# Kernel tuning notes

Hardware: AMD Instinct MI355X
Metric: run time of the kernel (lower is better)

Reference implementation:

```python
import jax, jax.numpy as jnp
import numpy as np

B, S, D, H = 2, 2048, 1024, 16
HD = D // H


def _linear_params(key, scale):
    kw, kb = jax.random.split(key)
    W = jax.random.normal(kw, (D, D), dtype=jnp.float32) * scale
    b = jax.random.normal(kb, (D,), dtype=jnp.float32) * scale
    return W, b


def setup_inputs() -> dict:
    key = jax.random.key(0)
    keys = jax.random.split(key, 10)
    scale = 1.0 / np.sqrt(D)
    vis = jax.random.normal(keys[0], (B, S, D), dtype=jnp.float32)
    inf = jax.random.normal(keys[1], (B, S, D), dtype=jnp.float32)
    names = ["q_vis", "k_vis", "v_vis", "q_inf", "k_inf", "v_inf", "o_vis", "o_inf"]
    out = {"vis": vis, "inf": inf}
    for n, k in zip(names, keys[2:]):
        W, b = _linear_params(k, scale)
        out["W_" + n] = W
        out["b_" + n] = b
    return out


def _heads(x):
    # [B,S,D] -> [B,H,S,HD]
    return x.reshape(B, S, H, HD).transpose(0, 2, 1, 3)


def _merge(x):
    # [B,H,S,HD] -> [B,S,D]
    return x.transpose(0, 2, 1, 3).reshape(B, S, D)


def reference(vis, inf, W_q_vis, b_q_vis, W_k_vis, b_k_vis, W_v_vis, b_v_vis,
              W_q_inf, b_q_inf, W_k_inf, b_k_inf, W_v_inf, b_v_inf,
              W_o_vis, b_o_vis, W_o_inf, b_o_inf):
    Qv = _heads(vis @ W_q_vis + b_q_vis)
    Kv = _heads(vis @ W_k_vis + b_k_vis)
    Vv = _heads(vis @ W_v_vis + b_v_vis)
    Qi = _heads(inf @ W_q_inf + b_q_inf)
    Ki = _heads(inf @ W_k_inf + b_k_inf)
    Vi = _heads(inf @ W_v_inf + b_v_inf)
    scale = 1.0 / jnp.sqrt(jnp.float32(HD))
    # vis queries attend over inf keys/values
    scores_vi = jnp.einsum("bhqd,bhkd->bhqk", Qv, Ki) * scale
    attn_inf = jax.nn.softmax(scores_vi, axis=-1)
    out_inf = jnp.einsum("bhqk,bhkd->bhqd", attn_inf, Vi)
    # inf queries attend over vis keys/values
    scores_iv = jnp.einsum("bhqd,bhkd->bhqk", Qi, Kv) * scale
    attn_vis = jax.nn.softmax(scores_iv, axis=-1)
    out_vis = jnp.einsum("bhqk,bhkd->bhqd", attn_vis, Vv)
    out_vis = _merge(out_vis) @ W_o_vis + b_o_vis
    out_inf = _merge(out_inf) @ W_o_inf + b_o_inf
    return (out_vis, out_inf)
```

## Files before the change

kernel.cpp:

```cpp
#include <hip/hip_runtime.h>
#include <hip/hip_bf16.h>

#define DEV __device__ __forceinline__

typedef __attribute__((ext_vector_type(4))) float f32x4;
typedef __attribute__((ext_vector_type(16))) float f32x16;
typedef __attribute__((ext_vector_type(8))) __bf16 bf16x8;
typedef __attribute__((ext_vector_type(8))) unsigned short ushort8;
typedef __attribute__((ext_vector_type(4))) unsigned int uint32x4;

static constexpr int BATCH = 2, SEQ = 2048, DM = 1024, NH = 16, HDIM = 64;
static constexpr size_t XSZ = (size_t)BATCH * SEQ * DM;

DEV unsigned short f2bf(float f) {
  union { float f; unsigned int u; } v; v.f = f;
  unsigned int r = (v.u + 0x7fffu + ((v.u >> 16) & 1u)) >> 16;
  return (unsigned short)r;
}

DEV bf16x8 ld8(const unsigned short* p) {
  return __builtin_bit_cast(bf16x8, *(const ushort8*)p);
}

DEV f32x4 mfma16(bf16x8 a, bf16x8 b, f32x4 c) {
  return __builtin_amdgcn_mfma_f32_16x16x32_bf16(a, b, c, 0, 0, 0);
}
DEV f32x16 mfma32(bf16x8 a, bf16x8 b, f32x16 c) {
  return __builtin_amdgcn_mfma_f32_32x32x16_bf16(a, b, c, 0, 0, 0);
}

DEV unsigned cvtpk(float lo, float hi) {
  unsigned r;
  asm("v_cvt_pk_bf16_f32 %0, %1, %2" : "=v"(r) : "v"(lo), "v"(hi));
  return r;
}
DEV void plswap(unsigned& a, unsigned& b) {
  asm("v_permlane32_swap_b32 %0, %1" : "+v"(a), "+v"(b));
}

DEV void gll16(const unsigned short* g, unsigned short* l) {
  __builtin_amdgcn_global_load_lds(
      (__attribute__((address_space(1))) void*)(unsigned short*)g,
      (__attribute__((address_space(3))) void*)l, 16, 0, 0);
}

__global__ __launch_bounds__(256)
void k_convert_x(const float* __restrict__ vis, const float* __restrict__ inff,
                 unsigned short* __restrict__ out) {
  const float* src = blockIdx.z ? inff : vis;
  unsigned short* dst = out + (size_t)blockIdx.z * XSZ;
  const size_t i = ((size_t)blockIdx.x * 256 + threadIdx.x) * 8;
  const float4 a = *(const float4*)(src + i);
  const float4 b = *(const float4*)(src + i + 4);
  ushort8 v;
  v[0] = f2bf(a.x); v[1] = f2bf(a.y); v[2] = f2bf(a.z); v[3] = f2bf(a.w);
  v[4] = f2bf(b.x); v[5] = f2bf(b.y); v[6] = f2bf(b.z); v[7] = f2bf(b.w);
  *(ushort8*)(dst + i) = v;
}

struct WPtrs { const float* w[8]; };

__global__ __launch_bounds__(256)
void k_convert_w(WPtrs p, unsigned short* __restrict__ wt) {
  const float* W = p.w[blockIdx.z];
  unsigned short* Wt = wt + (size_t)blockIdx.z * (1024 * 1024);
  const int k0 = blockIdx.y * 64, n0 = blockIdx.x * 64;
  __shared__ unsigned short t[64][68];
  const int tx = threadIdx.x & 15, ty = threadIdx.x >> 4;
#pragma unroll
  for (int i = 0; i < 4; ++i) {
    const int kr = ty * 4 + i;
    const float4 v = *(const float4*)(W + (size_t)(k0 + kr) * 1024 + n0 + tx * 4);
    t[kr][tx * 4 + 0] = f2bf(v.x); t[kr][tx * 4 + 1] = f2bf(v.y);
    t[kr][tx * 4 + 2] = f2bf(v.z); t[kr][tx * 4 + 3] = f2bf(v.w);
  }
  __syncthreads();
#pragma unroll
  for (int i = 0; i < 4; ++i) {
    const int nr = ty * 4 + i;
    ushort4 o;
    o.x = t[tx * 4 + 0][nr]; o.y = t[tx * 4 + 1][nr];
    o.z = t[tx * 4 + 2][nr]; o.w = t[tx * 4 + 3][nr];
    *(ushort4*)(Wt + (size_t)(n0 + nr) * 1024 + k0 + tx * 4) = o;
  }
}

struct GemmJob { const unsigned short* A; const unsigned short* W;
                 const float* bias; void* out; float scale; int mode; };
struct GemmJobs { GemmJob j[6]; };

__global__ __launch_bounds__(256)
void k_gemm(GemmJobs jobs) {
  const GemmJob jb = jobs.j[blockIdx.z];
  const int lane = threadIdx.x & 63, w = threadIdx.x >> 6;
  const int wr = w >> 1, wc = w & 1;
  const int r = lane & 15, g = lane >> 4;

  const int nid = blockIdx.x + (blockIdx.y << 3);
  const int bxs = nid >> 5;
  const int bys = ((nid & 7) << 2) + ((nid >> 3) & 3);
  const int bm = bys * 128, bn = bxs * 128;

  __shared__ __align__(16) unsigned short As[128 * 64];
  __shared__ __align__(16) unsigned short Bs[128 * 64];

  const int srow = lane >> 3;
  const int schunk = (lane & 7) ^ srow;
  const unsigned short* Ag = jb.A + (size_t)(bm + w * 32 + srow) * DM + schunk * 8;
  const unsigned short* Bg = jb.W + (size_t)(bn + w * 32 + srow) * DM + schunk * 8;

  f32x4 acc[4][4] = {};

  for (int kt = 0; kt < DM; kt += 64) {
#pragma unroll
    for (int j = 0; j < 4; ++j) {
      gll16(Ag + kt + j * 8 * DM, As + (w * 4 + j) * 512);
      gll16(Bg + kt + j * 8 * DM, Bs + (w * 4 + j) * 512);
    }
    __syncthreads();
#pragma unroll
    for (int kk = 0; kk < 2; ++kk) {
      bf16x8 a[4], b[4];
#pragma unroll
      for (int m = 0; m < 4; ++m) {
        const int row = wr * 64 + m * 16 + r;
        const int pos = (kk * 4 + g) ^ (row & 7);
        a[m] = ld8(As + row * 64 + pos * 8);
      }
#pragma unroll
      for (int n = 0; n < 4; ++n) {
        const int row = wc * 64 + n * 16 + r;
        const int pos = (kk * 4 + g) ^ (row & 7);
        b[n] = ld8(Bs + row * 64 + pos * 8);
      }
#pragma unroll
      for (int m = 0; m < 4; ++m)
#pragma unroll
        for (int n = 0; n < 4; ++n)
          acc[m][n] = mfma16(a[m], b[n], acc[m][n]);
    }
    __syncthreads();
  }

  if (jb.mode == 0) {
    unsigned short* O = (unsigned short*)jb.out;
#pragma unroll
    for (int n = 0; n < 4; ++n) {
      const int nc = bn + wc * 64 + n * 16 + r;
      const float bv = jb.bias[nc];
      const int h = nc >> 6, hd = nc & 63;
#pragma unroll
      for (int m = 0; m < 4; ++m)
#pragma unroll
        for (int i = 0; i < 4; ++i) {
          const int mr = bm + wr * 64 + m * 16 + g * 4 + i;
          const int bb = mr >> 11, s = mr & 2047;
          O[((size_t)(bb * NH + h) * SEQ + s) * HDIM + hd] =
              f2bf((acc[m][n][i] + bv) * jb.scale);
        }
    }
  } else if (jb.mode == 2) {
    unsigned short* O = (unsigned short*)jb.out;
#pragma unroll
    for (int n = 0; n < 4; ++n) {
      const int nc = bn + wc * 64 + n * 16 + r;
      const float bv = jb.bias[nc];
      const int h = nc >> 6, hd = nc & 63;
#pragma unroll
      for (int m = 0; m < 4; ++m) {
        const int mr = bm + wr * 64 + m * 16 + g * 4;
        const int bb = mr >> 11, s = mr & 2047;
        ushort4 pv;
        pv.x = f2bf(acc[m][n][0] + bv);
        pv.y = f2bf(acc[m][n][1] + bv);
        pv.z = f2bf(acc[m][n][2] + bv);
        pv.w = f2bf(acc[m][n][3] + bv);
        *(ushort4*)(O + ((size_t)(bb * NH + h) * HDIM + hd) * SEQ + s) = pv;
      }
    }
  } else {
    float* O = (float*)jb.out;
#pragma unroll
    for (int n = 0; n < 4; ++n) {
      const int nc = bn + wc * 64 + n * 16 + r;
      const float bv = jb.bias[nc];
#pragma unroll
      for (int m = 0; m < 4; ++m)
#pragma unroll
        for (int i = 0; i < 4; ++i) {
          const int mr = bm + wr * 64 + m * 16 + g * 4 + i;
          O[(size_t)mr * DM + nc] = acc[m][n][i] + bv;
        }
    }
  }
}

struct AttnJob { const unsigned short* Q; const unsigned short* K;
                 const unsigned short* Vt; unsigned short* O; };
struct AttnJobs { AttnJob j[2]; };

__global__ __launch_bounds__(512, 4)
void k_attn(AttnJobs jobs) {
  const AttnJob jb = jobs.j[blockIdx.z];
  const int nid = blockIdx.x + (blockIdx.y << 3);
  const int qt = nid >> 5;
  const int bh = ((nid & 7) << 2) + ((nid >> 3) & 3);
  const int lane = threadIdx.x & 63, w = threadIdx.x >> 6;
  const int q5 = lane & 31, hi = lane >> 5;
  const int qrow = qt * 256 + w * 32 + q5;

  const unsigned short* Qp = jb.Q + (size_t)bh * SEQ * HDIM;
  const unsigned short* Kp = jb.K + (size_t)bh * SEQ * HDIM;
  const unsigned short* Vp = jb.Vt + (size_t)bh * HDIM * SEQ;

  __shared__ __align__(16) unsigned short Ks[3][64 * 64];
  __shared__ __align__(16) unsigned short Vs[3][64 * 64];

  bf16x8 qf[4];
#pragma unroll
  for (int c = 0; c < 4; ++c)
    qf[c] = ld8(Qp + (size_t)qrow * HDIM + c * 16 + hi * 8);

  const int srow = w * 8 + (lane >> 3);
  const int schunk = (lane & 7) ^ (srow & 7);
  const unsigned short* Kg = Kp + (size_t)srow * HDIM + schunk * 8;
  const unsigned short* Vg = Vp + (size_t)srow * SEQ + schunk * 8;

  auto stage = [&](int buf, int kv0) {
    gll16(Kg + (size_t)kv0 * HDIM, Ks[buf] + w * 512);
    gll16(Vg + kv0,                Vs[buf] + w * 512);
  };

  f32x16 o0 = {}, o1 = {};
  float mrow = -1e30f, lrow = 0.f;
  const int swz = q5 & 7;
  constexpr int NT = SEQ / 64;

  stage(0, 0);
  stage(1, 64);
  asm volatile("s_waitcnt vmcnt(2)" ::: "memory");
  __builtin_amdgcn_s_barrier();
  __builtin_amdgcn_sched_barrier(0);

  int cur = 0, sb = 2;
  for (int t = 0; t < NT; ++t) {
    if (t + 2 < NT) stage(sb, (t + 2) * 64);

    f32x16 s0 = {}, s1 = {};
    __builtin_amdgcn_s_setprio(1);
#pragma unroll
    for (int c = 0; c < 4; ++c) {
      const int sl = ((2 * c + hi) ^ swz) * 8;
      s0 = mfma32(ld8(Ks[cur] + q5 * 64 + sl), qf[c], s0);
      s1 = mfma32(ld8(Ks[cur] + (32 + q5) * 64 + sl), qf[c], s1);
    }
    __builtin_amdgcn_s_setprio(0);

    float tm[8];
#pragma unroll
    for (int r = 0; r < 8; ++r)
      tm[r] = fmaxf(fmaxf(s0[r], s0[r + 8]), fmaxf(s1[r], s1[r + 8]));
    float mx = fmaxf(fmaxf(fmaxf(tm[0], tm[1]), tm[2]),
                     fmaxf(fmaxf(tm[3], tm[4]), fmaxf(fmaxf(tm[5], tm[6]), tm[7])));
    mx = fmaxf(mx, __shfl_xor(mx, 32, 64));

    if (!__all(mx <= mrow + 11.5416f)) {
      const float mn = fmaxf(mx, mrow);
      const float al = __builtin_amdgcn_exp2f(mrow - mn);
      mrow = mn;
      lrow *= al;
#pragma unroll
      for (int r = 0; r < 16; ++r) { o0[r] *= al; o1[r] *= al; }
    }

    float ps0 = 0.f, ps1 = 0.f;
#pragma unroll
    for (int r = 0; r < 16; ++r) {
      s0[r] = __builtin_amdgcn_exp2f(s0[r] - mrow); ps0 += s0[r];
      s1[r] = __builtin_amdgcn_exp2f(s1[r] - mrow); ps1 += s1[r];
    }
    lrow += ps0 + ps1;

    unsigned pk0[8], pk1[8];
#pragma unroll
    for (int ww = 0; ww < 8; ++ww) {
      pk0[ww] = cvtpk(s0[2 * ww], s0[2 * ww + 1]);
      pk1[ww] = cvtpk(s1[2 * ww], s1[2 * ww + 1]);
    }

    __builtin_amdgcn_s_setprio(1);
#pragma unroll
    for (int c = 0; c < 4; ++c) {
      const int wb = 4 * (c & 1);
      unsigned a0 = (c < 2) ? pk0[wb + 0] : pk1[wb + 0];
      unsigned a1 = (c < 2) ? pk0[wb + 1] : pk1[wb + 1];
      unsigned b0 = (c < 2) ? pk0[wb + 2] : pk1[wb + 2];
      unsigned b1 = (c < 2) ? pk0[wb + 3] : pk1[wb + 3];
      plswap(a0, b0);
      plswap(a1, b1);
      uint32x4 fw = {a0, a1, b0, b1};
      const bf16x8 pf = __builtin_bit_cast(bf16x8, fw);
      const int sl = ((2 * c + hi) ^ swz) * 8;
      o0 = mfma32(ld8(Vs[cur] + q5 * 64 + sl), pf, o0);
      o1 = mfma32(ld8(Vs[cur] + (32 + q5) * 64 + sl), pf, o1);
    }
    __builtin_amdgcn_s_setprio(0);

    if (t + 1 < NT) {
      if (t + 2 < NT) {
        asm volatile("s_waitcnt vmcnt(2)" ::: "memory");
      } else {
        asm volatile("s_waitcnt vmcnt(0)" ::: "memory");
      }
      __builtin_amdgcn_s_barrier();
      __builtin_amdgcn_sched_barrier(0);
    }
    sb = cur;
    cur = (cur == 2) ? 0 : cur + 1;
  }

  const float ltot = lrow + __shfl_xor(lrow, 32, 64);
  const float inv = 1.f / ltot;
  const int bb = bh >> 4, h = bh & 15;
  unsigned short* Ob = jb.O + ((size_t)bb * SEQ + qrow) * DM + h * HDIM;

  auto storeO = [&](const f32x16 oo, int dbase) {
#pragma unroll
    for (int g4 = 0; g4 < 4; ++g4) {
      ushort4 pv;
      pv.x = f2bf(oo[4 * g4 + 0] * inv);
      pv.y = f2bf(oo[4 * g4 + 1] * inv);
      pv.z = f2bf(oo[4 * g4 + 2] * inv);
      pv.w = f2bf(oo[4 * g4 + 3] * inv);
      *(ushort4*)(Ob + dbase + 8 * g4 + 4 * hi) = pv;
    }
  };
  storeO(o0, 0);
  storeO(o1, 32);
}

extern "C" void kernel_launch(void* const* d_in, const int* in_sizes, int n_in,
                              void* d_out, int out_size, void* d_ws, size_t ws_size,
                              hipStream_t stream) {
  const float* vis = (const float*)d_in[0];
  const float* inff = (const float*)d_in[1];

  unsigned short* xbf  = (unsigned short*)d_ws;
  unsigned short* wt   = xbf + 2 * XSZ;
  unsigned short* Qv   = wt + (size_t)8 * 1024 * 1024;
  unsigned short* Kv   = Qv + XSZ;
  unsigned short* Vv   = Kv + XSZ;
  unsigned short* Qi   = Vv + XSZ;
  unsigned short* Ki   = Qi + XSZ;
  unsigned short* Vi   = Ki + XSZ;
  unsigned short* Vvt  = Vi + XSZ;
  unsigned short* Vit  = Vvt + XSZ;
  unsigned short* atA  = Vit + XSZ;
  unsigned short* atB  = atA + XSZ;

  k_convert_x<<<dim3(2048, 1, 2), 256, 0, stream>>>(vis, inff, xbf);

  WPtrs wp;
  wp.w[0] = (const float*)d_in[2];  wp.w[1] = (const float*)d_in[4];
  wp.w[2] = (const float*)d_in[6];  wp.w[3] = (const float*)d_in[8];
  wp.w[4] = (const float*)d_in[10]; wp.w[5] = (const float*)d_in[12];
  wp.w[6] = (const float*)d_in[14]; wp.w[7] = (const float*)d_in[16];
  k_convert_w<<<dim3(16, 16, 8), 256, 0, stream>>>(wp, wt);

  const size_t WSZ = (size_t)1024 * 1024;
  const float qsc = 0.18033688011f;
  GemmJobs pj;
  pj.j[0] = { xbf,       wt + 0 * WSZ, (const float*)d_in[3],  (void*)Qv,  qsc, 0 };
  pj.j[1] = { xbf,       wt + 1 * WSZ, (const float*)d_in[5],  (void*)Kv,  1.f, 0 };
  pj.j[2] = { xbf,       wt + 2 * WSZ, (const float*)d_in[7],  (void*)Vvt, 1.f, 2 };
  pj.j[3] = { xbf + XSZ, wt + 3 * WSZ, (const float*)d_in[9],  (void*)Qi,  qsc, 0 };
  pj.j[4] = { xbf + XSZ, wt + 4 * WSZ, (const float*)d_in[11], (void*)Ki,  1.f, 0 };
  pj.j[5] = { xbf + XSZ, wt + 5 * WSZ, (const float*)d_in[13], (void*)Vit, 1.f, 2 };
  k_gemm<<<dim3(8, 32, 6), 256, 0, stream>>>(pj);

  AttnJobs aj;
  aj.j[0] = { Qv, Ki, Vit, atA };
  aj.j[1] = { Qi, Kv, Vvt, atB };
  k_attn<<<dim3(8, 32, 2), 512, 0, stream>>>(aj);

  GemmJobs oj;
  oj.j[0] = { atB, wt + 6 * WSZ, (const float*)d_in[15], d_out, 1.f, 1 };
  oj.j[1] = { atA, wt + 7 * WSZ, (const float*)d_in[17], (void*)((float*)d_out + XSZ), 1.f, 1 };
  for (int z = 2; z < 6; ++z) oj.j[z] = oj.j[0];
  k_gemm<<<dim3(8, 32, 2), 256, 0, stream>>>(oj);
}
```

Before: 303.8 us.

## Replace GEMM with 256x256-tile double-buffered pipelined kernel and grid swizzle

The 128x128 single-buffered GEMM (256 threads) is replaced by a 256x256-tile kernel with 512 threads and two LDS buffers for each operand half. The next K-tile's loads are staged during compute, and each 64-wide K step is split into four phases separated by barriers and raised MFMA priority. A new block-index swizzle spreads jobs across the grid. This aims for more data reuse and overlap of global loads with MFMA, but the grid shrinks to 384 blocks for the projections and 128 for the output GEMM, which may underfill the CUs, and the register pressure from the accumulators rises.

```diff
diff --git a/kernel.cpp b/kernel.cpp
--- a/kernel.cpp
+++ b/kernel.cpp
@@ -89,57 +89,98 @@
                  const float* bias; void* out; float scale; int mode; };
 struct GemmJobs { GemmJob j[6]; };
 
-__global__ __launch_bounds__(256)
-void k_gemm(GemmJobs jobs) {
-  const GemmJob jb = jobs.j[blockIdx.z];
+__global__ __launch_bounds__(512, 2)
+void k_gemm256(GemmJobs jobs) {
   const int lane = threadIdx.x & 63, w = threadIdx.x >> 6;
-  const int wr = w >> 1, wc = w & 1;
+  const int wr = w >> 2, wc = w & 3;
   const int r = lane & 15, g = lane >> 4;
 
-  const int nid = blockIdx.x + (blockIdx.y << 3);
-  const int bxs = nid >> 5;
-  const int bys = ((nid & 7) << 2) + ((nid >> 3) & 3);
-  const int bm = bys * 128, bn = bxs * 128;
-
-  __shared__ __align__(16) unsigned short As[128 * 64];
-  __shared__ __align__(16) unsigned short Bs[128 * 64];
-
-  const int srow = lane >> 3;
-  const int schunk = (lane & 7) ^ srow;
-  const unsigned short* Ag = jb.A + (size_t)(bm + w * 32 + srow) * DM + schunk * 8;
-  const unsigned short* Bg = jb.W + (size_t)(bn + w * 32 + srow) * DM + schunk * 8;
-
-  f32x4 acc[4][4] = {};
-
-  for (int kt = 0; kt < DM; kt += 64) {
-#pragma unroll
-    for (int j = 0; j < 4; ++j) {
-      gll16(Ag + kt + j * 8 * DM, As + (w * 4 + j) * 512);
-      gll16(Bg + kt + j * 8 * DM, Bs + (w * 4 + j) * 512);
-    }
-    __syncthreads();
-#pragma unroll
-    for (int kk = 0; kk < 2; ++kk) {
-      bf16x8 a[4], b[4];
-#pragma unroll
-      for (int m = 0; m < 4; ++m) {
-        const int row = wr * 64 + m * 16 + r;
-        const int pos = (kk * 4 + g) ^ (row & 7);
-        a[m] = ld8(As + row * 64 + pos * 8);
-      }
-#pragma unroll
-      for (int n = 0; n < 4; ++n) {
-        const int row = wc * 64 + n * 16 + r;
-        const int pos = (kk * 4 + g) ^ (row & 7);
-        b[n] = ld8(Bs + row * 64 + pos * 8);
-      }
-#pragma unroll
-      for (int m = 0; m < 4; ++m)
-#pragma unroll
-        for (int n = 0; n < 4; ++n)
-          acc[m][n] = mfma16(a[m], b[n], acc[m][n]);
-    }
-    __syncthreads();
+  const int lin = blockIdx.x + (blockIdx.y << 2) + ((blockIdx.z * 16) << 2);
+  const int q = gridDim.z << 3;
+  const int swz = (lin & 7) * q + (lin >> 3);
+  const int bxs = swz & 3, bys = (swz >> 2) & 15, bzs = swz >> 6;
+  const GemmJob jb = jobs.j[bzs];
+  const int bm = bys * 256, bn = bxs * 256;
+
+  __shared__ __align__(16) unsigned short L[2][2][2][8192];
+
+  const int uu = ((lane & 7) ^ (lane >> 3)) * 8;
+  const int rb = w * 8 + (lane >> 3);
+
+  auto stage = [&](int d_, int ab, int h, int tt) {
+#pragma unroll
+    for (int j = 0; j < 2; ++j) {
+      const int R = h * 128 + j * 64 + rb;
+      const unsigned short* src = (ab ? jb.W : jb.A)
+          + (size_t)((ab ? bn : bm) + R) * DM + tt * 64 + uu;
+      gll16(src, &L[d_][ab][h][(j * 8 + w) * 512]);
+    }
+  };
+
+  f32x4 acc[8][4] = {};
+  constexpr int NKT = DM / 64;
+
+  stage(0, 0, 0, 0); stage(0, 0, 1, 0); stage(0, 1, 0, 0); stage(0, 1, 1, 0);
+  stage(1, 1, 0, 1); stage(1, 1, 1, 1);
+  asm volatile("s_waitcnt vmcnt(4)" ::: "memory");
+  __builtin_amdgcn_s_barrier();
+  __builtin_amdgcn_sched_barrier(0);
+
+  const int px0 = (g ^ (r & 7)) * 8, px1 = ((4 + g) ^ (r & 7)) * 8;
+
+  for (int t = 0; t < NKT; ++t) {
+    const int d = t & 1;
+    const unsigned short* Ab = &L[d][0][wr][0];
+    const unsigned short* Bb = &L[d][1][wc >> 1][0];
+    bf16x8 bfr[4][2];
+
+#pragma unroll
+    for (int p = 0; p < 4; ++p) {
+      if (p == 0) {
+#pragma unroll
+        for (int n = 0; n < 4; ++n) {
+          const int rowl = (wc & 1) * 64 + n * 16 + r;
+          bfr[n][0] = ld8(Bb + rowl * 64 + px0);
+          bfr[n][1] = ld8(Bb + rowl * 64 + px1);
+        }
+      }
+      bf16x8 af[2][2];
+#pragma unroll
+      for (int m2 = 0; m2 < 2; ++m2) {
+        const int rowl = (2 * p + m2) * 16 + r;
+        af[m2][0] = ld8(Ab + rowl * 64 + px0);
+        af[m2][1] = ld8(Ab + rowl * 64 + px1);
+      }
+      if (p == 0 && t + 1 < NKT) stage(d ^ 1, 0, 0, t + 1);
+      if (p == 1 && t + 1 < NKT) stage(d ^ 1, 0, 1, t + 1);
+      if (p == 2 && t + 2 < NKT) stage(d, 1, 0, t + 2);
+      if (p == 3 && t + 2 < NKT) stage(d, 1, 1, t + 2);
+
+      __builtin_amdgcn_s_barrier();
+      asm volatile("s_waitcnt lgkmcnt(0)" ::: "memory");
+      __builtin_amdgcn_sched_barrier(0);
+
+      __builtin_amdgcn_s_setprio(1);
+#pragma unroll
+      for (int m2 = 0; m2 < 2; ++m2) {
+        const int mm = 2 * p + m2;
+#pragma unroll
+        for (int n = 0; n < 4; ++n) {
+          acc[mm][n] = mfma16(af[m2][0], bfr[n][0], acc[mm][n]);
+          acc[mm][n] = mfma16(af[m2][1], bfr[n][1], acc[mm][n]);
+        }
+      }
+      __builtin_amdgcn_s_setprio(0);
+
+      if (p < 3) {
+        __builtin_amdgcn_s_barrier();
+      } else if (t + 1 < NKT) {
+        if (t + 2 < NKT) asm volatile("s_waitcnt vmcnt(4)" ::: "memory");
+        else             asm volatile("s_waitcnt vmcnt(0)" ::: "memory");
+        __builtin_amdgcn_s_barrier();
+        __builtin_amdgcn_sched_barrier(0);
+      }
+    }
   }
 
   if (jb.mode == 0) {
@@ -150,10 +191,10 @@
       const float bv = jb.bias[nc];
       const int h = nc >> 6, hd = nc & 63;
 #pragma unroll
-      for (int m = 0; m < 4; ++m)
+      for (int m = 0; m < 8; ++m)
 #pragma unroll
         for (int i = 0; i < 4; ++i) {
-          const int mr = bm + wr * 64 + m * 16 + g * 4 + i;
+          const int mr = bm + wr * 128 + m * 16 + g * 4 + i;
           const int bb = mr >> 11, s = mr & 2047;
           O[((size_t)(bb * NH + h) * SEQ + s) * HDIM + hd] =
               f2bf((acc[m][n][i] + bv) * jb.scale);
@@ -167,8 +208,8 @@
       const float bv = jb.bias[nc];
       const int h = nc >> 6, hd = nc & 63;
 #pragma unroll
-      for (int m = 0; m < 4; ++m) {
-        const int mr = bm + wr * 64 + m * 16 + g * 4;
+      for (int m = 0; m < 8; ++m) {
+        const int mr = bm + wr * 128 + m * 16 + g * 4;
         const int bb = mr >> 11, s = mr & 2047;
         ushort4 pv;
         pv.x = f2bf(acc[m][n][0] + bv);
@@ -185,10 +226,10 @@
       const int nc = bn + wc * 64 + n * 16 + r;
       const float bv = jb.bias[nc];
 #pragma unroll
-      for (int m = 0; m < 4; ++m)
+      for (int m = 0; m < 8; ++m)
 #pragma unroll
         for (int i = 0; i < 4; ++i) {
-          const int mr = bm + wr * 64 + m * 16 + g * 4 + i;
+          const int mr = bm + wr * 128 + m * 16 + g * 4 + i;
           O[(size_t)mr * DM + nc] = acc[m][n][i] + bv;
         }
     }
@@ -233,7 +274,7 @@
 
   f32x16 o0 = {}, o1 = {};
   float mrow = -1e30f, lrow = 0.f;
-  const int swz = q5 & 7;
+  const int swzl = q5 & 7;
   constexpr int NT = SEQ / 64;
 
   stage(0, 0);
@@ -250,7 +291,7 @@
     __builtin_amdgcn_s_setprio(1);
 #pragma unroll
     for (int c = 0; c < 4; ++c) {
-      const int sl = ((2 * c + hi) ^ swz) * 8;
+      const int sl = ((2 * c + hi) ^ swzl) * 8;
       s0 = mfma32(ld8(Ks[cur] + q5 * 64 + sl), qf[c], s0);
       s1 = mfma32(ld8(Ks[cur] + (32 + q5) * 64 + sl), qf[c], s1);
     }
@@ -258,8 +299,8 @@
 
     float tm[8];
 #pragma unroll
-    for (int r = 0; r < 8; ++r)
-      tm[r] = fmaxf(fmaxf(s0[r], s0[r + 8]), fmaxf(s1[r], s1[r + 8]));
+    for (int rr = 0; rr < 8; ++rr)
+      tm[rr] = fmaxf(fmaxf(s0[rr], s0[rr + 8]), fmaxf(s1[rr], s1[rr + 8]));
     float mx = fmaxf(fmaxf(fmaxf(tm[0], tm[1]), tm[2]),
                      fmaxf(fmaxf(tm[3], tm[4]), fmaxf(fmaxf(tm[5], tm[6]), tm[7])));
     mx = fmaxf(mx, __shfl_xor(mx, 32, 64));
@@ -270,14 +311,14 @@
       mrow = mn;
       lrow *= al;
 #pragma unroll
-      for (int r = 0; r < 16; ++r) { o0[r] *= al; o1[r] *= al; }
+      for (int rr = 0; rr < 16; ++rr) { o0[rr] *= al; o1[rr] *= al; }
     }
 
     float ps0 = 0.f, ps1 = 0.f;
 #pragma unroll
-    for (int r = 0; r < 16; ++r) {
-      s0[r] = __builtin_amdgcn_exp2f(s0[r] - mrow); ps0 += s0[r];
-      s1[r] = __builtin_amdgcn_exp2f(s1[r] - mrow); ps1 += s1[r];
+    for (int rr = 0; rr < 16; ++rr) {
+      s0[rr] = __builtin_amdgcn_exp2f(s0[rr] - mrow); ps0 += s0[rr];
+      s1[rr] = __builtin_amdgcn_exp2f(s1[rr] - mrow); ps1 += s1[rr];
     }
     lrow += ps0 + ps1;
 
@@ -300,7 +341,7 @@
       plswap(a1, b1);
       uint32x4 fw = {a0, a1, b0, b1};
       const bf16x8 pf = __builtin_bit_cast(bf16x8, fw);
-      const int sl = ((2 * c + hi) ^ swz) * 8;
+      const int sl = ((2 * c + hi) ^ swzl) * 8;
       o0 = mfma32(ld8(Vs[cur] + q5 * 64 + sl), pf, o0);
       o1 = mfma32(ld8(Vs[cur] + (32 + q5) * 64 + sl), pf, o1);
     }
@@ -376,7 +417,7 @@
   pj.j[3] = { xbf + XSZ, wt + 3 * WSZ, (const float*)d_in[9],  (void*)Qi,  qsc, 0 };
   pj.j[4] = { xbf + XSZ, wt + 4 * WSZ, (const float*)d_in[11], (void*)Ki,  1.f, 0 };
   pj.j[5] = { xbf + XSZ, wt + 5 * WSZ, (const float*)d_in[13], (void*)Vit, 1.f, 2 };
-  k_gemm<<<dim3(8, 32, 6), 256, 0, stream>>>(pj);
+  k_gemm256<<<dim3(4, 16, 6), 512, 0, stream>>>(pj);
 
   AttnJobs aj;
   aj.j[0] = { Qv, Ki, Vit, atA };
@@ -387,5 +428,5 @@
   oj.j[0] = { atB, wt + 6 * WSZ, (const float*)d_in[15], d_out, 1.f, 1 };
   oj.j[1] = { atA, wt + 7 * WSZ, (const float*)d_in[17], (void*)((float*)d_out + XSZ), 1.f, 1 };
   for (int z = 2; z < 6; ++z) oj.j[z] = oj.j[0];
-  k_gemm<<<dim3(8, 32, 2), 256, 0, stream>>>(oj);
-}
+  k_gemm256<<<dim3(4, 16, 2), 512, 0, stream>>>(oj);
+}
```

Measured after the change: 320.6 us. 5.5% more time.
